# Optimization experiments

Hardware: AMD Instinct MI355X
Metric: run time of the kernel (lower is better)

Reference implementation:

```python
import jax, jax.numpy as jnp
import numpy as np

D_MODEL = 1024
N_HEAD = 16
SEQ_LEN = 4096


def setup_inputs() -> dict:
    key = jax.random.key(0)
    ks = jax.random.split(key, 5)
    s = 0.02
    return {
        "x": jax.random.normal(ks[0], (SEQ_LEN, D_MODEL), dtype=jnp.float32),
        "w_qkv": jax.random.normal(ks[1], (D_MODEL, 3 * D_MODEL), dtype=jnp.float32) * s,
        "b_qkv": jnp.zeros((3 * D_MODEL,), dtype=jnp.float32),
        "w_o": jax.random.normal(ks[2], (D_MODEL, D_MODEL), dtype=jnp.float32) * s,
        "b_o": jnp.zeros((D_MODEL,), dtype=jnp.float32),
    }


def reference(x, w_qkv, b_qkv, w_o, b_o):
    seq_len, d_model = x.shape
    n_head = N_HEAD
    d_h = d_model // n_head

    qkv = x @ w_qkv + b_qkv                                  # [S, 3D]
    q, k, v = jnp.split(qkv, 3, axis=-1)                     # each [S, D]
    # [S, D] -> [H, S, d_h]
    q = q.reshape(seq_len, n_head, d_h).transpose(1, 0, 2)
    k = k.reshape(seq_len, n_head, d_h).transpose(1, 0, 2)
    v = v.reshape(seq_len, n_head, d_h).transpose(1, 0, 2)

    sim = jnp.einsum("hsd,htd->hst", q, k) / jnp.sqrt(jnp.float32(d_h))  # [H, S, S]
    causal = jnp.tril(jnp.ones((seq_len, seq_len), dtype=bool))[None]    # [1, S, S]
    neg_inf = jnp.finfo(sim.dtype).min
    sim = jnp.where(causal, sim, neg_inf)
    attn = jax.nn.softmax(sim, axis=-1)                                  # [H, S, S]
    out = jnp.einsum("hst,htd->hsd", attn, v)                            # [H, S, d_h]
    out = out.transpose(1, 0, 2).reshape(seq_len, d_model)               # [S, D]
    return out @ w_o + b_o
```

## Files before the change

kernel.cpp:

```cpp
#include <hip/hip_runtime.h>
#include <hip/hip_bf16.h>
#include <stdint.h>

typedef __bf16 bf16_t;
typedef __bf16 bf16x8 __attribute__((ext_vector_type(8)));
typedef float f32x4 __attribute__((ext_vector_type(4)));
typedef float f32x16 __attribute__((ext_vector_type(16)));

#define SEQ_LEN 4096
#define D_MODEL 1024
#define N_HEAD 16



__device__ __forceinline__ void gload_lds16(const void* g, void* lds) {
  __builtin_amdgcn_global_load_lds(
      (__attribute__((address_space(1))) void*)(g),
      (__attribute__((address_space(3))) void*)(lds), 16, 0, 0);
}

__device__ __forceinline__ unsigned short f2bfu(float f) {
  __bf16 h = (__bf16)f;
  return __builtin_bit_cast(unsigned short, h);
}

__device__ __forceinline__ unsigned cvt_pk_bf16(float a, float b) {
  unsigned r;
  asm("v_cvt_pk_bf16_f32 %0, %1, %2" : "=v"(r) : "v"(a), "v"(b));
  return r;
}


__global__ __launch_bounds__(256) void cvt_f32_bf16(const float* __restrict__ in,
                                                    bf16_t* __restrict__ out, int n) {
  int i = (blockIdx.x * 256 + threadIdx.x) * 4;
  if (i < n) {
    float4 v = *(const float4*)(in + i);
    unsigned int lo = (unsigned)f2bfu(v.x) | ((unsigned)f2bfu(v.y) << 16);
    unsigned int hi = (unsigned)f2bfu(v.z) | ((unsigned)f2bfu(v.w) << 16);
    uint2 pk; pk.x = lo; pk.y = hi;
    *(uint2*)(out + i) = pk;
  }
}

__global__ __launch_bounds__(256) void transpose_cvt(const float* __restrict__ W,
                                                     bf16_t* __restrict__ Wt,
                                                     int R, int C) {
  __shared__ float tile[64][65];
  const int tc = C >> 6;
  const int bc = blockIdx.x % tc;
  const int br = blockIdx.x / tc;
  #pragma unroll
  for (int p = 0; p < 16; ++p) {
    int idx = p * 256 + threadIdx.x;
    int i = idx >> 6, j = idx & 63;
    tile[i][j] = W[(size_t)(br * 64 + i) * C + bc * 64 + j];
  }
  __syncthreads();
  #pragma unroll
  for (int p = 0; p < 16; ++p) {
    int idx = p * 256 + threadIdx.x;
    int jj = idx >> 6, ii = idx & 63;
    Wt[(size_t)(bc * 64 + jj) * R + br * 64 + ii] = (bf16_t)tile[ii][jj];
  }
}


template <bool OUT_BF16, bool VSPLIT>
__global__ __launch_bounds__(256) void gemm_bt(const bf16_t* __restrict__ A,
                                               const bf16_t* __restrict__ Bt,
                                               const float* __restrict__ bias,
                                               void* __restrict__ Cout,
                                               bf16_t* __restrict__ kfout,
                                               bf16_t* __restrict__ vfout,
                                               int M, int N, int K) {
  __shared__ bf16_t As[128 * 32];
  __shared__ bf16_t Bs[128 * 32];
  const int tid = threadIdx.x;
  const int lane = tid & 63;
  const int w = tid >> 6;
  const int wr = (w >> 1) * 64;
  const int wc = (w & 1) * 64;
  const int i16 = lane & 15;
  const int g = lane >> 4;
  const int ntn = N >> 7;
  const int bm = blockIdx.x / ntn;
  const int bn = blockIdx.x % ntn;
  const bf16_t* Abase = A + (size_t)(bm * 128) * K;
  const bf16_t* Bbase = Bt + (size_t)(bn * 128) * K;

  f32x4 acc[4][4];
  #pragma unroll
  for (int m = 0; m < 4; ++m)
    #pragma unroll
    for (int n = 0; n < 4; ++n)
      acc[m][n] = (f32x4){0.f, 0.f, 0.f, 0.f};

  for (int kt = 0; kt < K; kt += 32) {
    __syncthreads();
    #pragma unroll
    for (int p = 0; p < 2; ++p) {
      int idx = p * 256 + tid;
      int row = idx >> 2, ch = idx & 3;
      gload_lds16(Abase + (size_t)row * K + kt + ch * 8, (char*)As + idx * 16);
      gload_lds16(Bbase + (size_t)row * K + kt + ch * 8, (char*)Bs + idx * 16);
    }
    __syncthreads();
    bf16x8 af[4], bq[4];
    #pragma unroll
    for (int m = 0; m < 4; ++m)
      af[m] = *(const bf16x8*)(As + (wr + m * 16 + i16) * 32 + g * 8);
    #pragma unroll
    for (int n = 0; n < 4; ++n)
      bq[n] = *(const bf16x8*)(Bs + (wc + n * 16 + i16) * 32 + g * 8);
    #pragma unroll
    for (int m = 0; m < 4; ++m)
      #pragma unroll
      for (int n = 0; n < 4; ++n)
        acc[m][n] = __builtin_amdgcn_mfma_f32_16x16x32_bf16(af[m], bq[n], acc[m][n], 0, 0, 0);
  }

  #pragma unroll
  for (int m = 0; m < 4; ++m) {
    #pragma unroll
    for (int n = 0; n < 4; ++n) {
      int col = bn * 128 + wc + n * 16 + i16;
      float bv = bias ? bias[col] : 0.f;
      int row0 = bm * 128 + wr + m * 16 + g * 4;
      if (VSPLIT) {
        if (col < 1024) {
          #pragma unroll
          for (int r = 0; r < 4; ++r)
            ((bf16_t*)Cout)[(size_t)(row0 + r) * 1024 + col] = (bf16_t)(acc[m][n][r] + bv);
        } else if (col < 2048) {
          const float sc = 0.18033688011112042f;
          int dg = col - 1024;
          int hh = dg >> 6, d = dg & 63;
          int ks = d >> 4, hib = (d >> 3) & 1, e = d & 7;
          int t = row0 >> 5, l0 = row0 & 31;
          bf16_t* kfp = kfout + (size_t)hh * 262144 + t * 2048 + ks * 512 +
                        hib * 256 + l0 * 8 + e;
          #pragma unroll
          for (int r = 0; r < 4; ++r)
            kfp[r * 8] = (bf16_t)((acc[m][n][r] + bv) * sc);
        } else {
          int dg = col - 2048;
          int hh = dg >> 6, dh = dg & 63;
          int dt = dh >> 5, l31v = dh & 31;
          int t = row0 >> 5, inner = row0 & 31;
          int g2 = inner >> 4, hiv = (inner >> 3) & 1, e0 = inner & 7;
          uint2 pk;
          pk.x = cvt_pk_bf16(acc[m][n][0] + bv, acc[m][n][1] + bv);
          pk.y = cvt_pk_bf16(acc[m][n][2] + bv, acc[m][n][3] + bv);
          *(uint2*)(vfout + (size_t)hh * 262144 + t * 2048 + dt * 1024 +
                    g2 * 512 + hiv * 256 + l31v * 8 + e0) = pk;
        }
      } else {
        #pragma unroll
        for (int r = 0; r < 4; ++r) {
          float v = acc[m][n][r] + bv;
          if (OUT_BF16)
            ((bf16_t*)Cout)[(size_t)(row0 + r) * N + col] = (bf16_t)v;
          else
            ((float*)Cout)[(size_t)(row0 + r) * N + col] = v;
        }
      }
    }
  }
}


__global__ __launch_bounds__(256) void attn_fwd(const bf16_t* __restrict__ qbuf,
                                                const bf16_t* __restrict__ kf,
                                                const bf16_t* __restrict__ vf,
                                                bf16_t* __restrict__ aout) {
  __shared__ float Obuf[2][32][68];
  __shared__ float lpart[4][2][32];
  const int tid = threadIdx.x;
  const int w = tid >> 6;
  const int lane = tid & 63;
  const int l31 = lane & 31;
  const int hi = lane >> 5;
  const int bid = blockIdx.x;
  const int h = ((bid & 7) << 1) | ((bid >> 3) & 1);
  const int j = 127 - (bid >> 4);
  const int qg0 = j * 32;
  const int q = qg0 + l31;

  bf16x8 qf[4];
  #pragma unroll
  for (int ks = 0; ks < 4; ++ks)
    qf[ks] = *(const bf16x8*)(qbuf + (size_t)q * 1024 + h * 64 + ks * 16 + hi * 8);

  const bf16_t* kp = kf + (size_t)h * 262144 + hi * 256 + l31 * 8;
  const bf16_t* vp = vf + (size_t)h * 262144 + hi * 256 + l31 * 8;

  f32x16 ot0, ot1;
  #pragma unroll
  for (int r = 0; r < 16; ++r) { ot0[r] = 0.f; ot1[r] = 0.f; }
  float l_run = 0.f;

  const int nt = j + 1;
  bf16x8 kc[4], kn[4], vc[4];
  #pragma unroll
  for (int ks = 0; ks < 4; ++ks) {
    kc[ks] = *(const bf16x8*)(kp + w * 2048 + ks * 512);
    kn[ks] = kc[ks];
  }

  for (int t = w; t < nt; t += 4) {
    #pragma unroll
    for (int i = 0; i < 4; ++i) {
      int dt = i >> 1, g2 = i & 1;
      vc[i] = *(const bf16x8*)(vp + (size_t)t * 2048 + dt * 1024 + g2 * 512);
    }
    if (t + 4 < nt) {
      #pragma unroll
      for (int ks = 0; ks < 4; ++ks)
        kn[ks] = *(const bf16x8*)(kp + (size_t)(t + 4) * 2048 + ks * 512);
    }

    f32x16 s;
    #pragma unroll
    for (int r = 0; r < 16; ++r) s[r] = 0.f;
    __builtin_amdgcn_s_setprio(1);
    #pragma unroll
    for (int ks = 0; ks < 4; ++ks)
      s = __builtin_amdgcn_mfma_f32_32x32x16_bf16(kc[ks], qf[ks], s, 0, 0, 0);
    __builtin_amdgcn_s_setprio(0);

    if (t == nt - 1) {
      #pragma unroll
      for (int r = 0; r < 16; ++r) {
        int c = (r & 3) + 8 * (r >> 2) + 4 * hi;
        if (c > l31) s[r] = -1e30f;
      }
    }

    #pragma unroll
    for (int r = 0; r < 16; ++r)
      s[r] = __builtin_amdgcn_exp2f(s[r]);

    float sm[8];
    #pragma unroll
    for (int r = 0; r < 8; ++r) sm[r] = s[r] + s[r + 8];
    #pragma unroll
    for (int r = 0; r < 4; ++r) sm[r] = sm[r] + sm[r + 4];
    l_run += (sm[0] + sm[1]) + (sm[2] + sm[3]);

    bf16x8 pb[2];
    #pragma unroll
    for (int g2 = 0; g2 < 2; ++g2) {
      const int r0 = g2 * 8;
      unsigned a0 = cvt_pk_bf16(s[r0 + 0], s[r0 + 1]);
      unsigned a1 = cvt_pk_bf16(s[r0 + 2], s[r0 + 3]);
      unsigned b0 = cvt_pk_bf16(s[r0 + 4], s[r0 + 5]);
      unsigned b1 = cvt_pk_bf16(s[r0 + 6], s[r0 + 7]);
      unsigned X0 = hi ? a0 : b0;
      unsigned X1 = hi ? a1 : b1;
      unsigned Y0 = __shfl_xor(X0, 32);
      unsigned Y1 = __shfl_xor(X1, 32);
      uint4 f;
      f.x = hi ? Y0 : a0;
      f.y = hi ? Y1 : a1;
      f.z = hi ? b0 : Y0;
      f.w = hi ? b1 : Y1;
      pb[g2] = __builtin_bit_cast(bf16x8, f);
    }

    __builtin_amdgcn_s_setprio(1);
    ot0 = __builtin_amdgcn_mfma_f32_32x32x16_bf16(vc[0], pb[0], ot0, 0, 0, 0);
    ot0 = __builtin_amdgcn_mfma_f32_32x32x16_bf16(vc[1], pb[1], ot0, 0, 0, 0);
    ot1 = __builtin_amdgcn_mfma_f32_32x32x16_bf16(vc[2], pb[0], ot1, 0, 0, 0);
    ot1 = __builtin_amdgcn_mfma_f32_32x32x16_bf16(vc[3], pb[1], ot1, 0, 0, 0);
    __builtin_amdgcn_s_setprio(0);

    #pragma unroll
    for (int ks = 0; ks < 4; ++ks) kc[ks] = kn[ks];
  }

  lpart[w][hi][l31] = l_run;
  if (w >= 2) {
    #pragma unroll
    for (int dt = 0; dt < 2; ++dt) {
      const f32x16& o = dt ? ot1 : ot0;
      #pragma unroll
      for (int rq = 0; rq < 4; ++rq) {
        f32x4 qd;
        qd[0] = o[4 * rq + 0];
        qd[1] = o[4 * rq + 1];
        qd[2] = o[4 * rq + 2];
        qd[3] = o[4 * rq + 3];
        *(f32x4*)&Obuf[w - 2][l31][dt * 32 + 8 * rq + 4 * hi] = qd;
      }
    }
  }
  __syncthreads();
  if (w < 2) {
    #pragma unroll
    for (int dt = 0; dt < 2; ++dt) {
      const f32x16& o = dt ? ot1 : ot0;
      #pragma unroll
      for (int rq = 0; rq < 4; ++rq) {
        f32x4 qd = *(const f32x4*)&Obuf[w][l31][dt * 32 + 8 * rq + 4 * hi];
        qd[0] += o[4 * rq + 0];
        qd[1] += o[4 * rq + 1];
        qd[2] += o[4 * rq + 2];
        qd[3] += o[4 * rq + 3];
        *(f32x4*)&Obuf[w][l31][dt * 32 + 8 * rq + 4 * hi] = qd;
      }
    }
  }
  __syncthreads();
  #pragma unroll
  for (int iter = 0; iter < 8; ++iter) {
    int qq = w * 8 + iter;
    float sum = Obuf[0][qq][lane] + Obuf[1][qq][lane];
    float lst = lpart[0][0][qq] + lpart[0][1][qq] + lpart[1][0][qq] + lpart[1][1][qq] +
                lpart[2][0][qq] + lpart[2][1][qq] + lpart[3][0][qq] + lpart[3][1][qq];
    aout[(size_t)(qg0 + qq) * 1024 + h * 64 + lane] = (bf16_t)(sum / lst);
  }
}


extern "C" void kernel_launch(void* const* d_in, const int* in_sizes, int n_in,
                              void* d_out, int out_size, void* d_ws, size_t ws_size,
                              hipStream_t stream) {
  const float* x     = (const float*)d_in[0];
  const float* w_qkv = (const float*)d_in[1];
  const float* b_qkv = (const float*)d_in[2];
  const float* w_o   = (const float*)d_in[3];
  const float* b_o   = (const float*)d_in[4];

  char* ws = (char*)d_ws;
  bf16_t* xh    = (bf16_t*)(ws);
  bf16_t* wqkvT = (bf16_t*)(ws + 8388608);
  bf16_t* woT   = (bf16_t*)(ws + 14680064);
  bf16_t* qbuf  = (bf16_t*)(ws + 16777216);
  bf16_t* kfb   = (bf16_t*)(ws + 25165824);
  bf16_t* vfb   = (bf16_t*)(ws + 33554432);
  bf16_t* aout  = (bf16_t*)(ws + 41943040);

  cvt_f32_bf16<<<(SEQ_LEN * D_MODEL) / 1024, 256, 0, stream>>>(x, xh, SEQ_LEN * D_MODEL);
  transpose_cvt<<<(1024 / 64) * (3072 / 64), 256, 0, stream>>>(w_qkv, wqkvT, 1024, 3072);
  transpose_cvt<<<(1024 / 64) * (1024 / 64), 256, 0, stream>>>(w_o, woT, 1024, 1024);

  gemm_bt<true, true><<<(4096 / 128) * (3072 / 128), 256, 0, stream>>>(
      xh, wqkvT, b_qkv, (void*)qbuf, kfb, vfb, 4096, 3072, 1024);

  attn_fwd<<<N_HEAD * (SEQ_LEN / 32), 256, 0, stream>>>(qbuf, kfb, vfb, aout);

  gemm_bt<false, false><<<(4096 / 128) * (1024 / 128), 256, 0, stream>>>(
      aout, woT, b_o, d_out, nullptr, nullptr, 4096, 1024, 1024);
}
```

Before: 142.1 us.

## Store Q in MFMA fragment layout and swizzle GEMM block order across XCDs

The QKV GEMM epilogue now writes Q in the same per-head, tile-packed fragment layout already used for K, with unit scale. The attention kernel can then load its Q fragments as contiguous 16-byte chunks instead of strided row reads. Both GEMMs also remap block indices with an 8-way swizzle (blockIdx&7 times nwg/8) so consecutive tiles land on the same XCD for better L2 reuse. The Q epilogue's scattered 2-byte stores may cost more than the previous row-major stores.

```diff
diff --git a/kernel.cpp b/kernel.cpp
--- a/kernel.cpp
+++ b/kernel.cpp
@@ -71,6 +71,7 @@
                                                const bf16_t* __restrict__ Bt,
                                                const float* __restrict__ bias,
                                                void* __restrict__ Cout,
+                                               bf16_t* __restrict__ qfout,
                                                bf16_t* __restrict__ kfout,
                                                bf16_t* __restrict__ vfout,
                                                int M, int N, int K) {
@@ -84,8 +85,10 @@
   const int i16 = lane & 15;
   const int g = lane >> 4;
   const int ntn = N >> 7;
-  const int bm = blockIdx.x / ntn;
-  const int bn = blockIdx.x % ntn;
+  const int nwg = gridDim.x;
+  const int bswz = (blockIdx.x & 7) * (nwg >> 3) + (blockIdx.x >> 3);
+  const int bm = bswz / ntn;
+  const int bn = bswz % ntn;
   const bf16_t* Abase = A + (size_t)(bm * 128) * K;
   const bf16_t* Bbase = Bt + (size_t)(bn * 128) * K;
 
@@ -128,21 +131,19 @@
       float bv = bias ? bias[col] : 0.f;
       int row0 = bm * 128 + wr + m * 16 + g * 4;
       if (VSPLIT) {
-        if (col < 1024) {
-          #pragma unroll
-          for (int r = 0; r < 4; ++r)
-            ((bf16_t*)Cout)[(size_t)(row0 + r) * 1024 + col] = (bf16_t)(acc[m][n][r] + bv);
-        } else if (col < 2048) {
-          const float sc = 0.18033688011112042f;
-          int dg = col - 1024;
+        if (col < 2048) {
+          const bool isK = (col >= 1024);
+          const float scl = isK ? 0.18033688011112042f : 1.0f;
+          bf16_t* base = isK ? kfout : qfout;
+          int dg = col & 1023;
           int hh = dg >> 6, d = dg & 63;
           int ks = d >> 4, hib = (d >> 3) & 1, e = d & 7;
           int t = row0 >> 5, l0 = row0 & 31;
-          bf16_t* kfp = kfout + (size_t)hh * 262144 + t * 2048 + ks * 512 +
-                        hib * 256 + l0 * 8 + e;
+          bf16_t* fp = base + (size_t)hh * 262144 + t * 2048 + ks * 512 +
+                       hib * 256 + l0 * 8 + e;
           #pragma unroll
           for (int r = 0; r < 4; ++r)
-            kfp[r * 8] = (bf16_t)((acc[m][n][r] + bv) * sc);
+            fp[r * 8] = (bf16_t)((acc[m][n][r] + bv) * scl);
         } else {
           int dg = col - 2048;
           int hh = dg >> 6, dh = dg & 63;
@@ -170,7 +171,7 @@
 }
 
 
-__global__ __launch_bounds__(256) void attn_fwd(const bf16_t* __restrict__ qbuf,
+__global__ __launch_bounds__(256) void attn_fwd(const bf16_t* __restrict__ qf_,
                                                 const bf16_t* __restrict__ kf,
                                                 const bf16_t* __restrict__ vf,
                                                 bf16_t* __restrict__ aout) {
@@ -185,12 +186,12 @@
   const int h = ((bid & 7) << 1) | ((bid >> 3) & 1);
   const int j = 127 - (bid >> 4);
   const int qg0 = j * 32;
-  const int q = qg0 + l31;
-
+
+  const bf16_t* qp = qf_ + (size_t)h * 262144 + (size_t)j * 2048 + hi * 256 + l31 * 8;
   bf16x8 qf[4];
   #pragma unroll
   for (int ks = 0; ks < 4; ++ks)
-    qf[ks] = *(const bf16x8*)(qbuf + (size_t)q * 1024 + h * 64 + ks * 16 + hi * 8);
+    qf[ks] = *(const bf16x8*)(qp + ks * 512);
 
   const bf16_t* kp = kf + (size_t)h * 262144 + hi * 256 + l31 * 8;
   const bf16_t* vp = vf + (size_t)h * 262144 + hi * 256 + l31 * 8;
@@ -336,7 +337,7 @@
   bf16_t* xh    = (bf16_t*)(ws);
   bf16_t* wqkvT = (bf16_t*)(ws + 8388608);
   bf16_t* woT   = (bf16_t*)(ws + 14680064);
-  bf16_t* qbuf  = (bf16_t*)(ws + 16777216);
+  bf16_t* qfb   = (bf16_t*)(ws + 16777216);
   bf16_t* kfb   = (bf16_t*)(ws + 25165824);
   bf16_t* vfb   = (bf16_t*)(ws + 33554432);
   bf16_t* aout  = (bf16_t*)(ws + 41943040);
@@ -346,10 +347,10 @@
   transpose_cvt<<<(1024 / 64) * (1024 / 64), 256, 0, stream>>>(w_o, woT, 1024, 1024);
 
   gemm_bt<true, true><<<(4096 / 128) * (3072 / 128), 256, 0, stream>>>(
-      xh, wqkvT, b_qkv, (void*)qbuf, kfb, vfb, 4096, 3072, 1024);
-
-  attn_fwd<<<N_HEAD * (SEQ_LEN / 32), 256, 0, stream>>>(qbuf, kfb, vfb, aout);
+      xh, wqkvT, b_qkv, nullptr, qfb, kfb, vfb, 4096, 3072, 1024);
+
+  attn_fwd<<<N_HEAD * (SEQ_LEN / 32), 256, 0, stream>>>(qfb, kfb, vfb, aout);
 
   gemm_bt<false, false><<<(4096 / 128) * (1024 / 128), 256, 0, stream>>>(
-      aout, woT, b_o, d_out, nullptr, nullptr, 4096, 1024, 1024);
-}
+      aout, woT, b_o, d_out, nullptr, nullptr, nullptr, 4096, 1024, 1024);
+}
```

New measurement: 141.0 us. No clear change (-0.8%).
